# Optimization experiments

Hardware: AMD Instinct MI355X
Metric: run time of the kernel (lower is better)

Reference implementation:

```python
import jax, jax.numpy as jnp
import numpy as np

B, T, I = 32, 512, 1024
H, HS = 8, 128  # n_heads, head_size; hidden = H*HS = 1024
LIM = 1.0 / np.sqrt(HS)


def setup_inputs() -> dict:
    key = jax.random.key(0)
    kx, kif, kzo, khh, kb = jax.random.split(key, 5)
    u = lambda k, shp: jax.random.uniform(k, shp, jnp.float32, -LIM, LIM)
    return {
        "xs": jax.random.normal(kx, (B, T, I), jnp.float32),
        "weight_if": u(kif, (H, 2 * HS, I)),
        "weight_zo": u(kzo, (H, 2 * HS, I)),
        "weight_hh": u(khh, (H, 4 * HS, HS)),
        "bias": u(kb, (H, 4 * HS)),
    }


def reference(xs, weight_if, weight_zo, weight_hh, bias):
    # xs: [B, T, I]. Scan the sLSTM cell over time, batched over B via einsum.
    b, t, _ = xs.shape
    n_heads, four_hs, head_size = weight_hh.shape

    def step(state, x):  # x: [B, I]
        h, c, m, n = state  # each [B, H, HS]
        if_lin = jnp.einsum('hki,bi->bhk', weight_if, x)  # [B, H, 2*HS]
        zo_lin = jnp.einsum('hki,bi->bhk', weight_zo, x)  # [B, H, 2*HS]
        lin = jnp.concatenate([if_lin, zo_lin], axis=2)
        lin = lin + jnp.einsum('hkd,bhd->bhk', weight_hh, h) + bias  # [B, H, 4*HS]
        i, f, z, o = jnp.split(lin, 4, axis=2)
        z = jnp.tanh(z)
        o = jax.nn.sigmoid(o)
        m_new = jnp.maximum(f + m, i)          # stabilizer
        i_e = jnp.exp(i - m_new)
        f_e = jnp.exp(f + m - m_new)
        c_new = f_e * c + i_e * z
        n_new = f_e * n + i_e
        h_new = o * (c_new / n_new)
        return (h_new, c_new, m_new, n_new), h_new.reshape(b, n_heads * head_size)

    init = tuple(jnp.zeros((b, n_heads, head_size), xs.dtype) for _ in range(4))
    _, hs = jax.lax.scan(step, init, jnp.swapaxes(xs, 0, 1))  # hs: [T, B, hidden]
    return jnp.swapaxes(hs, 0, 1)  # [B, T, hidden]
```

## Files before the change

kernel.cpp:

```cpp
#include <hip/hip_runtime.h>
#include <hip/hip_bf16.h>
#include <stdint.h>

#define B_SZ 32
#define T_SZ 512
#define I_SZ 1024
#define H_SZ 8
#define HS_SZ 128

typedef __attribute__((ext_vector_type(8))) short short8;
typedef __attribute__((ext_vector_type(4))) float f32x4;

static __device__ __forceinline__ unsigned short f2bf(float f) {
  union { float f; unsigned int u; } c; c.f = f;
  unsigned int u = c.u;
  unsigned int r = (u + 0x7fffu + ((u >> 16) & 1u)) >> 16;
  return (unsigned short)r;
}
static __device__ __forceinline__ float bf2f(unsigned short s) {
  union { unsigned int u; float f; } c; c.u = ((unsigned int)s) << 16;
  return c.f;
}
static __device__ __forceinline__ void split2(float x, unsigned short& hi,
                                              unsigned short& lo) {
  hi = f2bf(x);
  lo = f2bf(x - bf2f(hi));
}

__global__ void conv_x_split(const float* __restrict__ x,
                             unsigned short* __restrict__ ohi,
                             unsigned short* __restrict__ olo, int n4) {
  int i = blockIdx.x * blockDim.x + threadIdx.x;
  if (i >= n4) return;
  float4 v = ((const float4*)x)[i];
  ushort4 h, l;
  split2(v.x, h.x, l.x);
  split2(v.y, h.y, l.y);
  split2(v.z, h.z, l.z);
  split2(v.w, h.w, l.w);
  ((ushort4*)ohi)[i] = h;
  ((ushort4*)olo)[i] = l;
}

__global__ void conv_w_split(const float* __restrict__ wif,
                             const float* __restrict__ wzo,
                             unsigned short* __restrict__ ohi,
                             unsigned short* __restrict__ olo) {
  int i = blockIdx.x * blockDim.x + threadIdx.x;
  int flat = i * 4;
  int n = flat >> 10;
  int col = flat & 1023;
  int h = n >> 9, k4 = n & 511;
  const float* src = (k4 < 256)
                         ? (wif + ((size_t)(h * 256 + k4) * 1024 + col))
                         : (wzo + ((size_t)(h * 256 + (k4 - 256)) * 1024 + col));
  float4 v = *(const float4*)src;
  ushort4 hh, ll;
  split2(v.x, hh.x, ll.x);
  split2(v.y, hh.y, ll.y);
  split2(v.z, hh.z, ll.z);
  split2(v.w, hh.w, ll.w);
  ((ushort4*)ohi)[i] = hh;
  ((ushort4*)olo)[i] = ll;
}

__device__ __forceinline__ void gld_lds16(const void* g, void* l) {
  __builtin_amdgcn_global_load_lds(
      (const __attribute__((address_space(1))) void*)g,
      (__attribute__((address_space(3))) void*)l, 16, 0, 0);
}

__global__ __launch_bounds__(256)
void gemm3_kernel(const unsigned short* __restrict__ Ahi,
                  const unsigned short* __restrict__ Alo,
                  const unsigned short* __restrict__ Whi,
                  const unsigned short* __restrict__ Wlo,
                  float* __restrict__ G, int t0, int ltch) {
  __shared__ short AH[128 * 32];
  __shared__ short AL[128 * 32];
  __shared__ short WH[128 * 32];
  __shared__ short WL[128 * 32];

  int tid = threadIdx.x;
  int lane = tid & 63, wave = tid >> 6;
  int wm = wave >> 1, wn = wave & 1;
  int bx = blockIdx.x, by = blockIdx.y;
  int l15 = lane & 15, kg = lane >> 4;
  int tchm = (1 << ltch) - 1;

  f32x4 zero4 = {0.f, 0.f, 0.f, 0.f};
  f32x4 acc[4][4];
#pragma unroll
  for (int mi = 0; mi < 4; ++mi)
#pragma unroll
    for (int ni = 0; ni < 4; ++ni) acc[mi][ni] = zero4;

  int u0 = wave * 128 + lane;
  int u1 = u0 + 64;
  int r0 = bx * 128 + (u0 >> 2);
  int r1 = bx * 128 + (u1 >> 2);
  size_t arow0 = (size_t)(r0 >> ltch) * 512 + t0 + (r0 & tchm);
  size_t arow1 = (size_t)(r1 >> ltch) * 512 + t0 + (r1 & tchm);
  size_t aoff0 = arow0 * 1024 + (u0 & 3) * 8;
  size_t aoff1 = arow1 * 1024 + (u1 & 3) * 8;
  size_t woff0 = (size_t)(by * 128 + (u0 >> 2)) * 1024 + (u0 & 3) * 8;
  size_t woff1 = (size_t)(by * 128 + (u1 >> 2)) * 1024 + (u1 & 3) * 8;

  short* ah_d0 = &AH[wave * 1024];
  short* ah_d1 = &AH[wave * 1024 + 512];
  short* al_d0 = &AL[wave * 1024];
  short* al_d1 = &AL[wave * 1024 + 512];
  short* wh_d0 = &WH[wave * 1024];
  short* wh_d1 = &WH[wave * 1024 + 512];
  short* wl_d0 = &WL[wave * 1024];
  short* wl_d1 = &WL[wave * 1024 + 512];

  for (int k0 = 0; k0 < 1024; k0 += 32) {
    __syncthreads();
    gld_lds16(Ahi + aoff0 + k0, ah_d0);
    gld_lds16(Ahi + aoff1 + k0, ah_d1);
    gld_lds16(Alo + aoff0 + k0, al_d0);
    gld_lds16(Alo + aoff1 + k0, al_d1);
    gld_lds16(Whi + woff0 + k0, wh_d0);
    gld_lds16(Whi + woff1 + k0, wh_d1);
    gld_lds16(Wlo + woff0 + k0, wl_d0);
    gld_lds16(Wlo + woff1 + k0, wl_d1);
    __syncthreads();

    short8 ah[4], al[4], wh[4], wl[4];
#pragma unroll
    for (int mi = 0; mi < 4; ++mi) {
      int ro = (wm * 64 + mi * 16 + l15) * 32 + kg * 8;
      ah[mi] = *(const short8*)&AH[ro];
      al[mi] = *(const short8*)&AL[ro];
    }
#pragma unroll
    for (int ni = 0; ni < 4; ++ni) {
      int ro = (wn * 64 + ni * 16 + l15) * 32 + kg * 8;
      wh[ni] = *(const short8*)&WH[ro];
      wl[ni] = *(const short8*)&WL[ro];
    }

#pragma unroll
    for (int mi = 0; mi < 4; ++mi)
#pragma unroll
      for (int ni = 0; ni < 4; ++ni) {
        acc[mi][ni] = __builtin_amdgcn_mfma_f32_16x16x32_bf16(
            ah[mi], wh[ni], acc[mi][ni], 0, 0, 0);
        acc[mi][ni] = __builtin_amdgcn_mfma_f32_16x16x32_bf16(
            ah[mi], wl[ni], acc[mi][ni], 0, 0, 0);
        acc[mi][ni] = __builtin_amdgcn_mfma_f32_16x16x32_bf16(
            al[mi], wh[ni], acc[mi][ni], 0, 0, 0);
      }
  }

#pragma unroll
  for (int mi = 0; mi < 4; ++mi)
#pragma unroll
    for (int ni = 0; ni < 4; ++ni)
#pragma unroll
      for (int r = 0; r < 4; ++r) {
        int grow = bx * 128 + wm * 64 + mi * 16 + kg * 4 + r;
        int gcol = by * 128 + wn * 64 + ni * 16 + l15;
        G[(size_t)grow * 4096 + gcol] = acc[mi][ni][r];
      }
}

__global__ __launch_bounds__(512, 1)
void recur_kernel(const float* __restrict__ G,
                  const float* __restrict__ Whh,
                  const float* __restrict__ bias,
                  float* __restrict__ out,
                  float* __restrict__ state,
                  int t0, int tch, int first) {
  int blk = blockIdx.x;
  int b = blk >> 3, h = blk & 7;
  int t = threadIdx.x;
  int w = t >> 6;
  int l = t & 63;
  int q = w >> 1;
  int em = (w & 1) * 64 + l;
  int eg = q * 32 + (l & 31);

  __shared__ __align__(16) float part[2][128 * 20];

  float wreg[128];
  {
    const float* wb = Whh + (size_t)h * 65536 + (size_t)q * 32;
#pragma unroll
    for (int g = 0; g < 4; ++g) {
      const float4* wp = (const float4*)(wb + (size_t)(g * 128 + em) * 128);
#pragma unroll
      for (int c4 = 0; c4 < 8; ++c4) {
        float4 v = wp[c4];
        wreg[g * 32 + c4 * 4 + 0] = v.x;
        wreg[g * 32 + c4 * 4 + 1] = v.y;
        wreg[g * 32 + c4 * 4 + 2] = v.z;
        wreg[g * 32 + c4 * 4 + 3] = v.w;
      }
    }
  }
#pragma unroll
  for (int i = 0; i < 128; ++i)
    asm volatile("" : "+v"(wreg[i]));

  int si = (b * 8 + h) * 128 + eg;
  float hreg = 0.f, c_r = 0.f, n_r = 0.f, m_r = 0.f;
  if (!first) {
    hreg = state[si];
    c_r = state[32768 + si];
    m_r = state[65536 + si];
    n_r = state[98304 + si];
  }
  float bj0 = bias[h * 512 + eg];
  float bj1 = bias[h * 512 + 128 + eg];
  float bj2 = bias[h * 512 + 256 + eg];
  float bj3 = bias[h * 512 + 384 + eg];

  const float* gpb = G + (size_t)(b * tch) * 4096 + h * 512 + eg;
  float* op = out + ((size_t)b * 512 + t0) * 1024 + h * 128 + eg;
  bool writer = ((w & 1) == 0) && (l < 32);

  int ebase = em * 20 + q * 4;
  int rb0 = eg * 20 + 0;
  int rb1 = eg * 20 + 4;
  int rb2 = eg * 20 + 8;
  int rb3 = eg * 20 + 12;

  float g0 = gpb[0], g1 = gpb[128], g2 = gpb[256], g3 = gpb[384];

  for (int s = 0; s < tch; ++s) {
    float gn0 = 0.f, gn1 = 0.f, gn2 = 0.f, gn3 = 0.f;
    if (s + 1 < tch) {
      const float* gr = gpb + (size_t)(s + 1) * 4096;
      gn0 = gr[0]; gn1 = gr[128]; gn2 = gr[256]; gn3 = gr[384];
    }

    float a0 = 0.f, a1 = 0.f, a2 = 0.f, a3 = 0.f;
    int hbits = __float_as_int(hreg);
#pragma unroll
    for (int c = 0; c < 32; ++c) {
      float hs = __int_as_float(__builtin_amdgcn_readlane(hbits, c));
      a0 = fmaf(wreg[c], hs, a0);
      a1 = fmaf(wreg[32 + c], hs, a1);
      a2 = fmaf(wreg[64 + c], hs, a2);
      a3 = fmaf(wreg[96 + c], hs, a3);
    }
    float4 pv = {a0, a1, a2, a3};
    *(float4*)&part[s & 1][ebase] = pv;
    __syncthreads();

    float4 p0 = *(const float4*)&part[s & 1][rb0];
    float4 p1 = *(const float4*)&part[s & 1][rb1];
    float4 p2 = *(const float4*)&part[s & 1][rb2];
    float4 p3 = *(const float4*)&part[s & 1][rb3];
    float iv = bj0 + g0 + ((p0.x + p1.x) + (p2.x + p3.x));
    float fv = bj1 + g1 + ((p0.y + p1.y) + (p2.y + p3.y));
    float zv = bj2 + g2 + ((p0.z + p1.z) + (p2.z + p3.z));
    float ov = bj3 + g3 + ((p0.w + p1.w) + (p2.w + p3.w));
    float e2 = __expf(2.f * zv);
    float zt = 1.f - 2.f * __builtin_amdgcn_rcpf(e2 + 1.f);
    float og = __builtin_amdgcn_rcpf(1.f + __expf(-ov));
    float mn = fmaxf(fv + m_r, iv);
    float ie = __expf(iv - mn);
    float fe = __expf(fv + m_r - mn);
    c_r = fe * c_r + ie * zt;
    n_r = fe * n_r + ie;
    m_r = mn;
    float hnew = og * c_r * __builtin_amdgcn_rcpf(n_r);
    hreg = hnew;
    if (writer) op[(size_t)s * 1024] = hnew;
    g0 = gn0; g1 = gn1; g2 = gn2; g3 = gn3;
  }

  if (writer) {
    state[si] = hreg;
    state[32768 + si] = c_r;
    state[65536 + si] = m_r;
    state[98304 + si] = n_r;
  }
}

extern "C" void kernel_launch(void* const* d_in, const int* in_sizes, int n_in,
                              void* d_out, int out_size, void* d_ws, size_t ws_size,
                              hipStream_t stream) {
  const float* xs   = (const float*)d_in[0];
  const float* wif  = (const float*)d_in[1];
  const float* wzo  = (const float*)d_in[2];
  const float* whh  = (const float*)d_in[3];
  const float* bias = (const float*)d_in[4];
  float* out = (float*)d_out;

  char* ws = (char*)d_ws;
  unsigned short* Ahi = (unsigned short*)ws;
  unsigned short* Alo = (unsigned short*)(ws + 33554432);
  unsigned short* Whi = (unsigned short*)(ws + 67108864);
  unsigned short* Wlo = (unsigned short*)(ws + 75497472);
  const size_t gbase = 83886080;

  int tch = 128;
  while (tch > 8 &&
         gbase + (size_t)32 * tch * 4096 * 4 + 524288 > ws_size)
    tch >>= 1;
  int ltch = (tch == 128) ? 7 : (tch == 64) ? 6 : (tch == 32) ? 5
             : (tch == 16) ? 4 : 3;

  float* G = (float*)(ws + gbase);
  float* state = (float*)(ws + gbase + (size_t)32 * tch * 4096 * 4);

  conv_x_split<<<16384, 256, 0, stream>>>(xs, Ahi, Alo, 4194304);
  conv_w_split<<<4096, 256, 0, stream>>>(wif, wzo, Whi, Wlo);

  for (int t0 = 0; t0 < 512; t0 += tch) {
    gemm3_kernel<<<dim3(tch / 4, 32), 256, 0, stream>>>(Ahi, Alo, Whi, Wlo,
                                                        G, t0, ltch);
    recur_kernel<<<256, 512, 0, stream>>>(G, whh, bias, out, state, t0, tch,
                                          t0 == 0);
  }
}
```

Measured before the change: 915.0 us.

## Double-buffer GEMM LDS loads, widen tile to 256 rows, swizzle LDS layout

The split-bf16 input-projection GEMM now uses 512-thread blocks covering 256 rows of A against 128 columns of W. Global-to-LDS loads go into two buffers, so the fetch for step k+2 overlaps compute on the current step. LDS rows are XOR-swizzled to reduce bank conflicts, and MFMA issue is grouped by operand with raised priority. The cost is more LDS per block (96KB) and fewer blocks, which risks lower occupancy and fragile manual waitcnt/barrier ordering.

Measured after the change: 822.1 us. -10.2%, faster.

```diff
diff --git a/kernel.cpp b/kernel.cpp
--- a/kernel.cpp
+++ b/kernel.cpp
@@ -70,23 +70,51 @@
       (__attribute__((address_space(3))) void*)l, 16, 0, 0);
 }
 
-__global__ __launch_bounds__(256)
+__global__ __launch_bounds__(512)
 void gemm3_kernel(const unsigned short* __restrict__ Ahi,
                   const unsigned short* __restrict__ Alo,
                   const unsigned short* __restrict__ Whi,
                   const unsigned short* __restrict__ Wlo,
                   float* __restrict__ G, int t0, int ltch) {
-  __shared__ short AH[128 * 32];
-  __shared__ short AL[128 * 32];
-  __shared__ short WH[128 * 32];
-  __shared__ short WL[128 * 32];
-
-  int tid = threadIdx.x;
-  int lane = tid & 63, wave = tid >> 6;
-  int wm = wave >> 1, wn = wave & 1;
-  int bx = blockIdx.x, by = blockIdx.y;
-  int l15 = lane & 15, kg = lane >> 4;
-  int tchm = (1 << ltch) - 1;
+  __shared__ short lds2[2][24576];
+
+  const int tid = threadIdx.x;
+  const int lane = tid & 63, wv = tid >> 6;
+  const int wm = wv >> 1, wn = wv & 1;
+  const int bx = blockIdx.x, by = blockIdx.y;
+  const int l15 = lane & 15, kg = lane >> 4;
+  const int tchm = (1 << ltch) - 1;
+
+  const unsigned short* gsrc[6];
+#pragma unroll
+  for (int t = 0; t < 6; ++t) {
+    int u = tid + t * 512;
+    int j = u & 3;
+    if (t < 4) {
+      int r = (u >> 2) & 255;
+      int gslot = j ^ ((r >> 1) & 3);
+      int cr = bx * 256 + r;
+      size_t xsrow = (size_t)(cr >> ltch) * 512 + t0 + (cr & tchm);
+      gsrc[t] = ((t < 2) ? Ahi : Alo) + xsrow * 1024 + gslot * 8;
+    } else {
+      int r = (u >> 2) & 127;
+      int gslot = j ^ ((r >> 1) & 3);
+      size_t wr = (size_t)by * 128 + r;
+      gsrc[t] = ((t == 4) ? Whi : Wlo) + wr * 1024 + gslot * 8;
+    }
+  }
+
+  int offa[4], offw[4];
+#pragma unroll
+  for (int mi = 0; mi < 4; ++mi) {
+    int r = wm * 64 + mi * 16 + l15;
+    offa[mi] = r * 32 + (kg ^ ((r >> 1) & 3)) * 8;
+  }
+#pragma unroll
+  for (int ni = 0; ni < 4; ++ni) {
+    int r = wn * 64 + ni * 16 + l15;
+    offw[ni] = r * 32 + (kg ^ ((r >> 1) & 3)) * 8;
+  }
 
   f32x4 zero4 = {0.f, 0.f, 0.f, 0.f};
   f32x4 acc[4][4];
@@ -95,63 +123,68 @@
 #pragma unroll
     for (int ni = 0; ni < 4; ++ni) acc[mi][ni] = zero4;
 
-  int u0 = wave * 128 + lane;
-  int u1 = u0 + 64;
-  int r0 = bx * 128 + (u0 >> 2);
-  int r1 = bx * 128 + (u1 >> 2);
-  size_t arow0 = (size_t)(r0 >> ltch) * 512 + t0 + (r0 & tchm);
-  size_t arow1 = (size_t)(r1 >> ltch) * 512 + t0 + (r1 & tchm);
-  size_t aoff0 = arow0 * 1024 + (u0 & 3) * 8;
-  size_t aoff1 = arow1 * 1024 + (u1 & 3) * 8;
-  size_t woff0 = (size_t)(by * 128 + (u0 >> 2)) * 1024 + (u0 & 3) * 8;
-  size_t woff1 = (size_t)(by * 128 + (u1 >> 2)) * 1024 + (u1 & 3) * 8;
-
-  short* ah_d0 = &AH[wave * 1024];
-  short* ah_d1 = &AH[wave * 1024 + 512];
-  short* al_d0 = &AL[wave * 1024];
-  short* al_d1 = &AL[wave * 1024 + 512];
-  short* wh_d0 = &WH[wave * 1024];
-  short* wh_d1 = &WH[wave * 1024 + 512];
-  short* wl_d0 = &WL[wave * 1024];
-  short* wl_d1 = &WL[wave * 1024 + 512];
-
-  for (int k0 = 0; k0 < 1024; k0 += 32) {
-    __syncthreads();
-    gld_lds16(Ahi + aoff0 + k0, ah_d0);
-    gld_lds16(Ahi + aoff1 + k0, ah_d1);
-    gld_lds16(Alo + aoff0 + k0, al_d0);
-    gld_lds16(Alo + aoff1 + k0, al_d1);
-    gld_lds16(Whi + woff0 + k0, wh_d0);
-    gld_lds16(Whi + woff1 + k0, wh_d1);
-    gld_lds16(Wlo + woff0 + k0, wl_d0);
-    gld_lds16(Wlo + woff1 + k0, wl_d1);
-    __syncthreads();
-
-    short8 ah[4], al[4], wh[4], wl[4];
-#pragma unroll
-    for (int mi = 0; mi < 4; ++mi) {
-      int ro = (wm * 64 + mi * 16 + l15) * 32 + kg * 8;
-      ah[mi] = *(const short8*)&AH[ro];
-      al[mi] = *(const short8*)&AL[ro];
-    }
-#pragma unroll
-    for (int ni = 0; ni < 4; ++ni) {
-      int ro = (wn * 64 + ni * 16 + l15) * 32 + kg * 8;
-      wh[ni] = *(const short8*)&WH[ro];
-      wl[ni] = *(const short8*)&WL[ro];
-    }
-
+#pragma unroll
+  for (int t = 0; t < 6; ++t)
+    gld_lds16(gsrc[t], &lds2[0][(wv * 64 + t * 512) * 8]);
+#pragma unroll
+  for (int t = 0; t < 6; ++t)
+    gld_lds16(gsrc[t] + 32, &lds2[1][(wv * 64 + t * 512) * 8]);
+  asm volatile("s_waitcnt vmcnt(6)" : : : "memory");
+  __builtin_amdgcn_s_barrier();
+
+  for (int ks = 0; ks < 32; ++ks) {
+    const short* bp = &lds2[ks & 1][0];
+
+    short8 ah[4], wh4[4], al[4], wl4[4];
+#pragma unroll
+    for (int mi = 0; mi < 4; ++mi) ah[mi] = *(const short8*)(bp + offa[mi]);
+#pragma unroll
+    for (int ni = 0; ni < 4; ++ni)
+      wh4[ni] = *(const short8*)(bp + 16384 + offw[ni]);
+
+    __builtin_amdgcn_s_setprio(1);
 #pragma unroll
     for (int mi = 0; mi < 4; ++mi)
 #pragma unroll
-      for (int ni = 0; ni < 4; ++ni) {
+      for (int ni = 0; ni < 4; ++ni)
         acc[mi][ni] = __builtin_amdgcn_mfma_f32_16x16x32_bf16(
-            ah[mi], wh[ni], acc[mi][ni], 0, 0, 0);
+            ah[mi], wh4[ni], acc[mi][ni], 0, 0, 0);
+
+#pragma unroll
+    for (int mi = 0; mi < 4; ++mi)
+      al[mi] = *(const short8*)(bp + 8192 + offa[mi]);
+#pragma unroll
+    for (int mi = 0; mi < 4; ++mi)
+#pragma unroll
+      for (int ni = 0; ni < 4; ++ni)
         acc[mi][ni] = __builtin_amdgcn_mfma_f32_16x16x32_bf16(
-            ah[mi], wl[ni], acc[mi][ni], 0, 0, 0);
+            al[mi], wh4[ni], acc[mi][ni], 0, 0, 0);
+
+#pragma unroll
+    for (int ni = 0; ni < 4; ++ni)
+      wl4[ni] = *(const short8*)(bp + 20480 + offw[ni]);
+#pragma unroll
+    for (int mi = 0; mi < 4; ++mi)
+#pragma unroll
+      for (int ni = 0; ni < 4; ++ni)
         acc[mi][ni] = __builtin_amdgcn_mfma_f32_16x16x32_bf16(
-            al[mi], wh[ni], acc[mi][ni], 0, 0, 0);
-      }
+            ah[mi], wl4[ni], acc[mi][ni], 0, 0, 0);
+    __builtin_amdgcn_s_setprio(0);
+
+    asm volatile("s_waitcnt lgkmcnt(0)" : : : "memory");
+    __builtin_amdgcn_sched_barrier(0);
+    __builtin_amdgcn_s_barrier();
+
+    if (ks + 2 < 32) {
+#pragma unroll
+      for (int t = 0; t < 6; ++t)
+        gld_lds16(gsrc[t] + (ks + 2) * 32,
+                  &lds2[ks & 1][(wv * 64 + t * 512) * 8]);
+      asm volatile("s_waitcnt vmcnt(6)" : : : "memory");
+    } else {
+      asm volatile("s_waitcnt vmcnt(0)" : : : "memory");
+    }
+    __builtin_amdgcn_s_barrier();
   }
 
 #pragma unroll
@@ -160,7 +193,7 @@
     for (int ni = 0; ni < 4; ++ni)
 #pragma unroll
       for (int r = 0; r < 4; ++r) {
-        int grow = bx * 128 + wm * 64 + mi * 16 + kg * 4 + r;
+        int grow = bx * 256 + wm * 64 + mi * 16 + kg * 4 + r;
         int gcol = by * 128 + wn * 64 + ni * 16 + l15;
         G[(size_t)grow * 4096 + gcol] = acc[mi][ni][r];
       }
@@ -312,8 +345,8 @@
   conv_w_split<<<4096, 256, 0, stream>>>(wif, wzo, Whi, Wlo);
 
   for (int t0 = 0; t0 < 512; t0 += tch) {
-    gemm3_kernel<<<dim3(tch / 4, 32), 256, 0, stream>>>(Ahi, Alo, Whi, Wlo,
-                                                        G, t0, ltch);
+    gemm3_kernel<<<dim3((32 * tch) / 256, 32), 512, 0, stream>>>(
+        Ahi, Alo, Whi, Wlo, G, t0, ltch);
     recur_kernel<<<256, 512, 0, stream>>>(G, whh, bias, out, state, t0, tch,
                                           t0 == 0);
   }
```
